# Kernel optimization log

Measured on AMD Instinct MI355X. Metric: run time of the kernel, lower is better.

## Reference

```python
import jax, jax.numpy as jnp
import numpy as np

EMBED_DIM = 1024
NUM_HEADS = 16
HEAD_DIM = EMBED_DIM // NUM_HEADS


def setup_inputs() -> dict:
    key = jax.random.key(0)
    ks = jax.random.split(key, 11)
    B, N, C = 2, 2048, EMBED_DIM
    s = 1.0 / np.sqrt(C)
    return {
        "query": jax.random.normal(ks[0], (B, N, C), jnp.float32),
        "key": jax.random.normal(ks[1], (B, N, C), jnp.float32),
        "value": jax.random.normal(ks[2], (B, N, C), jnp.float32),
        # torch nn.Linear weights: [out_features, in_features]
        "Wq": jax.random.normal(ks[3], (C, C), jnp.float32) * s,
        "bq": jnp.zeros((C,), jnp.float32),
        "Wk": jax.random.normal(ks[4], (C, C), jnp.float32) * s,
        "bk": jnp.zeros((C,), jnp.float32),
        "Wv": jax.random.normal(ks[5], (C, C), jnp.float32) * s,
        "bv": jnp.zeros((C,), jnp.float32),
        "Wo": jax.random.normal(ks[6], (C, C), jnp.float32) * s,
        "bo": jnp.zeros((C,), jnp.float32),
    }


def reference(query, key, value, Wq, bq, Wk, bk, Wv, bv, Wo, bo):
    B, N, C = query.shape
    H, D = NUM_HEADS, HEAD_DIM
    # projections (torch Linear: x @ W.T + b)
    q = query @ Wq.T + bq
    k = key @ Wk.T + bk
    v = value @ Wv.T + bv
    # [B, N, C] -> [B, H, N, D]
    q = q.reshape(B, N, H, D).transpose(0, 2, 1, 3)
    k = k.reshape(B, N, H, D).transpose(0, 2, 1, 3)
    v = v.reshape(B, N, H, D).transpose(0, 2, 1, 3)
    # scores: [B, H, N, N]
    scores = jnp.einsum("bhqd,bhkd->bhqk", q, k) / jnp.sqrt(jnp.asarray(D, q.dtype))
    attn = jax.nn.softmax(scores, axis=-1)
    # attend: [B, H, N, D] -> [B, N, C]
    out = jnp.einsum("bhqk,bhkd->bhqd", attn, v)
    out = out.transpose(0, 2, 1, 3).reshape(B, N, C)
    return out @ Wo.T + bo
```

## Files before the change

kernel.cpp:

```cpp
#include <hip/hip_runtime.h>
#include <hip/hip_bf16.h>
#include <cstdint>

typedef short bf16x8 __attribute__((ext_vector_type(8)));
typedef float f32x4 __attribute__((ext_vector_type(4)));
typedef float f32x16 __attribute__((ext_vector_type(16)));
typedef uint32_t u32x4v __attribute__((ext_vector_type(4)));
typedef unsigned short u16;

#define BATCH 2
#define NTOK 2048
#define CDIM 1024
#define NHEAD 16
#define DHEAD 64
#define MROWS 4096
#define KDIM 1024
#define KVB 128
#define NT (NTOK / KVB)

__device__ __forceinline__ uint32_t packbf2(float lo, float hi) {
    float2 f; f.x = lo; f.y = hi;
    __hip_bfloat162 h = __float22bfloat162_rn(f);
    uint32_t r;
    __builtin_memcpy(&r, &h, 4);
    return r;
}

__device__ __forceinline__ u16 f2bf(float x) {
    return (u16)(packbf2(x, 0.f) & 0xffffu);
}

__device__ __forceinline__ void gload_lds16(const void* g, void* l) {
    __builtin_amdgcn_global_load_lds((const __attribute__((address_space(1))) void*)g,
                                     (__attribute__((address_space(3))) void*)l,
                                     16, 0, 0);
}

__global__ __launch_bounds__(256) void cast_kernel(
    const float* __restrict__ q, const float* __restrict__ k, const float* __restrict__ v,
    const float* __restrict__ wq, const float* __restrict__ wk, const float* __restrict__ wv,
    const float* __restrict__ wo, u16* __restrict__ dst) {
    const size_t TOT = 16u << 20;
    size_t i0 = ((size_t)blockIdx.x * 256 + threadIdx.x) * 4;
    size_t stride = (size_t)gridDim.x * 256 * 4;
    for (size_t i = i0; i < TOT; i += stride) {
        const float* src;
        size_t off = i;
        if (i < (4u << 20))        { src = q;  }
        else if (i < (8u << 20))   { src = k;  off = i - (4u << 20); }
        else if (i < (12u << 20))  { src = v;  off = i - (8u << 20); }
        else if (i < (13u << 20))  { src = wq; off = i - (12u << 20); }
        else if (i < (14u << 20))  { src = wk; off = i - (13u << 20); }
        else if (i < (15u << 20))  { src = wv; off = i - (14u << 20); }
        else                       { src = wo; off = i - (15u << 20); }
        float4 f = *(const float4*)(src + off);
        uint2 packed;
        packed.x = packbf2(f.x, f.y);
        packed.y = packbf2(f.z, f.w);
        *(uint2*)(dst + i) = packed;
    }
}

__global__ __launch_bounds__(256, 3) void gemm_qkv(
    const u16* __restrict__ Xq, const u16* __restrict__ Xk, const u16* __restrict__ Xv,
    const u16* __restrict__ Wq, const u16* __restrict__ Wk, const u16* __restrict__ Wv,
    const float* __restrict__ bq, const float* __restrict__ bk, const float* __restrict__ bv,
    u16* __restrict__ Qo, u16* __restrict__ Ko, u16* __restrict__ Vo) {
    __shared__ u16 sA[128 * 32];
    __shared__ u16 sB[128 * 32];
    const int tid = threadIdx.x;
    const int lane = tid & 63;
    const int wave = tid >> 6;
    const int z = blockIdx.z;
    const u16* A  = (z == 0) ? Xq : (z == 1) ? Xk : Xv;
    const u16* Bw = (z == 0) ? Wq : (z == 1) ? Wk : Wv;
    const float* bias = (z == 0) ? bq : (z == 1) ? bk : bv;
    u16* Out = (z == 0) ? Qo : (z == 1) ? Ko : Vo;
    const float scale = (z == 0) ? 0.125f * 1.44269504088896f : 1.0f;

    const int m0 = blockIdx.x * 128, n0 = blockIdx.y * 128;
    const int wm = (wave >> 1) * 64, wn = (wave & 1) * 64;
    f32x4 acc[4][4] = {};
    const int rsel = lane & 15;
    const int ksel = (lane >> 4) * 8;

    for (int k0 = 0; k0 < KDIM; k0 += 32) {
#pragma unroll
        for (int u = 0; u < 2; ++u) {
            int c = tid + u * 256;
            int row = c >> 2, cin = c & 3;
            gload_lds16(A + (size_t)(m0 + row) * KDIM + k0 + cin * 8, &sA[c * 8]);
            gload_lds16(Bw + (size_t)(n0 + row) * KDIM + k0 + cin * 8, &sB[c * 8]);
        }
        __syncthreads();
        bf16x8 af[4], bfr[4];
#pragma unroll
        for (int i = 0; i < 4; ++i)
            af[i] = *(const bf16x8*)&sA[(wm + i * 16 + rsel) * 32 + ksel];
#pragma unroll
        for (int j = 0; j < 4; ++j)
            bfr[j] = *(const bf16x8*)&sB[(wn + j * 16 + rsel) * 32 + ksel];
#pragma unroll
        for (int i = 0; i < 4; ++i)
#pragma unroll
            for (int j = 0; j < 4; ++j)
                acc[i][j] = __builtin_amdgcn_mfma_f32_16x16x32_bf16(af[i], bfr[j], acc[i][j], 0, 0, 0);
        __syncthreads();
    }

    if (z != 2) {
#pragma unroll
        for (int i = 0; i < 4; ++i) {
            int mbase = m0 + wm + i * 16 + (lane >> 4) * 4;
#pragma unroll
            for (int j = 0; j < 4; ++j) {
                int n = n0 + wn + j * 16 + (lane & 15);
                float bv2 = bias[n];
                int h = n >> 6, d = n & 63;
#pragma unroll
                for (int r = 0; r < 4; ++r) {
                    int m = mbase + r;
                    int b = m >> 11, tok = m & 2047;
                    Out[(((size_t)(b * NHEAD + h)) * NTOK + tok) * DHEAD + d] =
                        f2bf((acc[i][j][r] + bv2) * scale);
                }
            }
        }
    } else {
#pragma unroll
        for (int i = 0; i < 4; ++i) {
            int mbase = m0 + wm + i * 16 + (lane >> 4) * 4;
            int b = mbase >> 11, tok = mbase & 2047;
#pragma unroll
            for (int j = 0; j < 4; ++j) {
                int n = n0 + wn + j * 16 + (lane & 15);
                float bv2 = bias[n];
                int h = n >> 6, d = n & 63;
                uint2 st;
                st.x = packbf2(acc[i][j][0] + bv2, acc[i][j][1] + bv2);
                st.y = packbf2(acc[i][j][2] + bv2, acc[i][j][3] + bv2);
                *(uint2*)&Out[(((size_t)(b * NHEAD + h)) * DHEAD + d) * NTOK + tok] = st;
            }
        }
    }
}

__global__ __launch_bounds__(256, 3) void gemm_out(
    const u16* __restrict__ A,
    const u16* __restrict__ Bw,
    const float* __restrict__ bias,
    float* __restrict__ Out,
    int M, int N, int K) {
    __shared__ u16 sA[128 * 32];
    __shared__ u16 sB[128 * 32];
    const int tid = threadIdx.x;
    const int lane = tid & 63;
    const int wave = tid >> 6;
    const int m0 = blockIdx.x * 128, n0 = blockIdx.y * 128;
    const int wm = (wave >> 1) * 64, wn = (wave & 1) * 64;
    f32x4 acc[4][4] = {};
    const int rsel = lane & 15;
    const int ksel = (lane >> 4) * 8;

    for (int k0 = 0; k0 < K; k0 += 32) {
#pragma unroll
        for (int u = 0; u < 2; ++u) {
            int c = tid + u * 256;
            int row = c >> 2, cin = c & 3;
            gload_lds16(A + (size_t)(m0 + row) * K + k0 + cin * 8, &sA[c * 8]);
            gload_lds16(Bw + (size_t)(n0 + row) * K + k0 + cin * 8, &sB[c * 8]);
        }
        __syncthreads();
        bf16x8 af[4], bfr[4];
#pragma unroll
        for (int i = 0; i < 4; ++i)
            af[i] = *(const bf16x8*)&sA[(wm + i * 16 + rsel) * 32 + ksel];
#pragma unroll
        for (int j = 0; j < 4; ++j)
            bfr[j] = *(const bf16x8*)&sB[(wn + j * 16 + rsel) * 32 + ksel];
#pragma unroll
        for (int i = 0; i < 4; ++i)
#pragma unroll
            for (int j = 0; j < 4; ++j)
                acc[i][j] = __builtin_amdgcn_mfma_f32_16x16x32_bf16(af[i], bfr[j], acc[i][j], 0, 0, 0);
        __syncthreads();
    }

#pragma unroll
    for (int i = 0; i < 4; ++i) {
        int mbase = m0 + wm + i * 16 + (lane >> 4) * 4;
#pragma unroll
        for (int j = 0; j < 4; ++j) {
            int n = n0 + wn + j * 16 + (lane & 15);
            float bv = bias[n];
#pragma unroll
            for (int r = 0; r < 4; ++r) {
                int m = mbase + r;
                Out[(size_t)m * N + n] = acc[i][j][r] + bv;
            }
        }
    }
}

__global__ __launch_bounds__(256, 2) void attn_kernel(
    const u16* __restrict__ Qg, const u16* __restrict__ Kg, const u16* __restrict__ Vg,
    u16* __restrict__ Og) {
    __shared__ u16 Ks[2][KVB * 64];
    __shared__ u16 Vt[2][64 * KVB];
    const int tid = threadIdx.x, lane = tid & 63, wave = tid >> 6;
    const int hi = lane >> 5, lq = lane & 31;

    int flat = blockIdx.x;
    int vflat = (flat & 7) * 64 + (flat >> 3);
    int bh = vflat >> 4;
    int qtile = vflat & 15;

    const int h = bh & (NHEAD - 1), b = bh >> 4;
    const u16* Qh = Qg + (size_t)bh * NTOK * DHEAD;
    const u16* Kh = Kg + (size_t)bh * NTOK * DHEAD;
    const u16* VhT = Vg + (size_t)bh * DHEAD * NTOK;
    const int qrow0 = qtile * 128 + wave * 32;
    const int qr = qrow0 + lq;

    bf16x8 qf[4];
#pragma unroll
    for (int dk = 0; dk < 4; ++dk)
        qf[dk] = *(const bf16x8*)&Qh[(size_t)qr * DHEAD + dk * 16 + hi * 8];

    f32x16 acc0 = {}, acc1 = {};
    f32x16 lacc = {};
    const bf16x8 ones = { (short)0x3F80, (short)0x3F80, (short)0x3F80, (short)0x3F80,
                          (short)0x3F80, (short)0x3F80, (short)0x3F80, (short)0x3F80 };

    const int pr = ((lq >> 2) & 1) * 8 + (lq & 3) + ((lq >> 3) & 1) * 4 + (lq >> 4) * 16;

    {
#pragma unroll
        for (int u = 0; u < 4; ++u) {
            int c2 = tid + u * 256;
            int kv = c2 >> 3, gi = c2 & 7;
            gload_lds16(Kh + (size_t)kv * DHEAD + (gi ^ (kv & 7)) * 8, &Ks[0][c2 * 8]);
        }
#pragma unroll
        for (int u = 0; u < 4; ++u) {
            int c2 = tid + u * 256;
            int d = c2 >> 4, gi = c2 & 15;
            gload_lds16(VhT + (size_t)d * NTOK + (gi ^ (d & 15)) * 8, &Vt[0][c2 * 8]);
        }
    }
    __syncthreads();

    int cur = 0;
    for (int t = 0; t < NT; ++t) {
        const bool pre = (t + 1 < NT);
        if (pre) {
#pragma unroll
            for (int u = 0; u < 4; ++u) {
                int c2 = tid + u * 256;
                int kv = c2 >> 3, gi = c2 & 7;
                gload_lds16(Kh + (size_t)((t + 1) * KVB + kv) * DHEAD + (gi ^ (kv & 7)) * 8,
                            &Ks[cur ^ 1][c2 * 8]);
            }
#pragma unroll
            for (int u = 0; u < 4; ++u) {
                int c2 = tid + u * 256;
                int d = c2 >> 4, gi = c2 & 15;
                gload_lds16(VhT + (size_t)d * NTOK + (t + 1) * KVB + (gi ^ (d & 15)) * 8,
                            &Vt[cur ^ 1][c2 * 8]);
            }
        }

        const char* kb_ = (const char*)&Ks[cur][0];
        bf16x8 pf[8];
#pragma unroll
        for (int j = 0; j < 4; ++j) {
            f32x16 T = {};
            int kv = j * 32 + pr;
            const char* kr = kb_ + kv * 128;
            int sx = (kv & 7) << 4;
#pragma unroll
            for (int dk = 0; dk < 4; ++dk) {
                bf16x8 kf = *(const bf16x8*)(kr + ((dk * 32 + hi * 16) ^ sx));
                T = __builtin_amdgcn_mfma_f32_32x32x16_bf16(kf, qf[dk], T, 0, 0, 0);
            }
#pragma unroll
            for (int i = 0; i < 16; ++i) T[i] = __builtin_amdgcn_exp2f(T[i]);
            u32x4v w0 = { packbf2(T[0], T[1]),  packbf2(T[2], T[3]),
                          packbf2(T[4], T[5]),  packbf2(T[6], T[7]) };
            u32x4v w1 = { packbf2(T[8], T[9]),  packbf2(T[10], T[11]),
                          packbf2(T[12], T[13]), packbf2(T[14], T[15]) };
            pf[j * 2]     = *(bf16x8*)&w0;
            pf[j * 2 + 1] = *(bf16x8*)&w1;
        }

        const char* vb_ = (const char*)&Vt[cur][0];
        __builtin_amdgcn_s_setprio(1);
#pragma unroll
        for (int db = 0; db < 2; ++db) {
            int d = db * 32 + lq;
#pragma unroll
            for (int ks = 0; ks < 8; ++ks) {
                int off = d * 256 + ((ks * 32 + hi * 16) ^ ((d & 15) << 4));
                bf16x8 vf = *(const bf16x8*)(vb_ + off);
                if (db == 0)
                    acc0 = __builtin_amdgcn_mfma_f32_32x32x16_bf16(vf, pf[ks], acc0, 0, 0, 0);
                else
                    acc1 = __builtin_amdgcn_mfma_f32_32x32x16_bf16(vf, pf[ks], acc1, 0, 0, 0);
            }
        }
#pragma unroll
        for (int ks = 0; ks < 8; ++ks)
            lacc = __builtin_amdgcn_mfma_f32_32x32x16_bf16(ones, pf[ks], lacc, 0, 0, 0);
        __builtin_amdgcn_s_setprio(0);

        __syncthreads();
        cur ^= 1;
    }

    float rinv = 1.0f / lacc[0];
#pragma unroll
    for (int db = 0; db < 2; ++db) {
#pragma unroll
        for (int rq = 0; rq < 4; ++rq) {
            int based = db * 32 + 8 * rq + 4 * hi;
            float o0, o1, o2, o3;
            if (db == 0) {
                o0 = acc0[rq * 4 + 0]; o1 = acc0[rq * 4 + 1];
                o2 = acc0[rq * 4 + 2]; o3 = acc0[rq * 4 + 3];
            } else {
                o0 = acc1[rq * 4 + 0]; o1 = acc1[rq * 4 + 1];
                o2 = acc1[rq * 4 + 2]; o3 = acc1[rq * 4 + 3];
            }
            uint2 st;
            st.x = packbf2(o0 * rinv, o1 * rinv);
            st.y = packbf2(o2 * rinv, o3 * rinv);
            *(uint2*)&Og[((size_t)(b * NTOK + qr)) * CDIM + h * DHEAD + based] = st;
        }
    }
}

extern "C" void kernel_launch(void* const* d_in, const int* in_sizes, int n_in,
                              void* d_out, int out_size, void* d_ws, size_t ws_size,
                              hipStream_t stream) {
    const float* q  = (const float*)d_in[0];
    const float* k  = (const float*)d_in[1];
    const float* v  = (const float*)d_in[2];
    const float* Wq = (const float*)d_in[3];
    const float* bq = (const float*)d_in[4];
    const float* Wk = (const float*)d_in[5];
    const float* bk = (const float*)d_in[6];
    const float* Wv = (const float*)d_in[7];
    const float* bv = (const float*)d_in[8];
    const float* Wo = (const float*)d_in[9];
    const float* bo = (const float*)d_in[10];

    u16* wsp = (u16*)d_ws;
    u16* Xq  = wsp;
    u16* Xk  = Xq + (4u << 20);
    u16* Xv  = Xk + (4u << 20);
    u16* Wqb = Xv + (4u << 20);
    u16* Wkb = Wqb + (1u << 20);
    u16* Wvb = Wkb + (1u << 20);
    u16* Wob = Wvb + (1u << 20);
    u16* Qb  = Wob + (1u << 20);
    u16* Kb  = Qb + (4u << 20);
    u16* Vb  = Kb + (4u << 20);
    u16* Ab  = Xq;

    cast_kernel<<<2048, 256, 0, stream>>>(q, k, v, Wq, Wk, Wv, Wo, Xq);

    gemm_qkv<<<dim3(MROWS / 128, CDIM / 128, 3), 256, 0, stream>>>(
        Xq, Xk, Xv, Wqb, Wkb, Wvb, bq, bk, bv, Qb, Kb, Vb);

    attn_kernel<<<512, 256, 0, stream>>>(Qb, Kb, Vb, Ab);

    gemm_out<<<dim3(MROWS / 128, CDIM / 128), 256, 0, stream>>>(
        Ab, Wob, bo, (float*)d_out, MROWS, CDIM, KDIM);
}
```

Measured before the change: 125.3 us.

## Switch attention to 16x16x32 MFMA with 64-row tiles and 64-key blocks

The attention kernel moves from 32x32x16 to 16x16x32 MFMA tiles. Each wave now handles 16 query rows instead of 32, the KV block shrinks from 128 to 64, and the grid doubles to 1024 blocks. The LDS swizzles are reworked to match, and launch bounds ask for 4 blocks per CU. This aims for more parallelism and occupancy with less register and LDS pressure per block, at the cost of more K/V reloads per query and more barriers per key sweep.

```diff
diff --git a/kernel.cpp b/kernel.cpp
--- a/kernel.cpp
+++ b/kernel.cpp
@@ -4,7 +4,6 @@
 
 typedef short bf16x8 __attribute__((ext_vector_type(8)));
 typedef float f32x4 __attribute__((ext_vector_type(4)));
-typedef float f32x16 __attribute__((ext_vector_type(16)));
 typedef uint32_t u32x4v __attribute__((ext_vector_type(4)));
 typedef unsigned short u16;
 
@@ -15,7 +14,7 @@
 #define DHEAD 64
 #define MROWS 4096
 #define KDIM 1024
-#define KVB 128
+#define KVB 64
 #define NT (NTOK / KVB)
 
 __device__ __forceinline__ uint32_t packbf2(float lo, float hi) {
@@ -202,50 +201,49 @@
     }
 }
 
-__global__ __launch_bounds__(256, 2) void attn_kernel(
+__global__ __launch_bounds__(256, 4) void attn_kernel(
     const u16* __restrict__ Qg, const u16* __restrict__ Kg, const u16* __restrict__ Vg,
     u16* __restrict__ Og) {
     __shared__ u16 Ks[2][KVB * 64];
     __shared__ u16 Vt[2][64 * KVB];
     const int tid = threadIdx.x, lane = tid & 63, wave = tid >> 6;
-    const int hi = lane >> 5, lq = lane & 31;
+    const int g = lane >> 4, m_ = lane & 15;
 
     int flat = blockIdx.x;
-    int vflat = (flat & 7) * 64 + (flat >> 3);
-    int bh = vflat >> 4;
-    int qtile = vflat & 15;
+    int vflat = (flat & 7) * 128 + (flat >> 3);
+    int bh = vflat >> 5;
+    int qtile = vflat & 31;
 
     const int h = bh & (NHEAD - 1), b = bh >> 4;
     const u16* Qh = Qg + (size_t)bh * NTOK * DHEAD;
     const u16* Kh = Kg + (size_t)bh * NTOK * DHEAD;
     const u16* VhT = Vg + (size_t)bh * DHEAD * NTOK;
-    const int qrow0 = qtile * 128 + wave * 32;
-    const int qr = qrow0 + lq;
-
-    bf16x8 qf[4];
-#pragma unroll
-    for (int dk = 0; dk < 4; ++dk)
-        qf[dk] = *(const bf16x8*)&Qh[(size_t)qr * DHEAD + dk * 16 + hi * 8];
-
-    f32x16 acc0 = {}, acc1 = {};
-    f32x16 lacc = {};
+    const int qrow0 = qtile * 64 + wave * 16;
+    const int qr = qrow0 + m_;
+
+    bf16x8 qf[2];
+#pragma unroll
+    for (int ks = 0; ks < 2; ++ks)
+        qf[ks] = *(const bf16x8*)&Qh[(size_t)qr * DHEAD + ks * 32 + g * 8];
+
+    f32x4 acc[4] = {};
+    f32x4 lacc = {};
     const bf16x8 ones = { (short)0x3F80, (short)0x3F80, (short)0x3F80, (short)0x3F80,
                           (short)0x3F80, (short)0x3F80, (short)0x3F80, (short)0x3F80 };
 
-    const int pr = ((lq >> 2) & 1) * 8 + (lq & 3) + ((lq >> 3) & 1) * 4 + (lq >> 4) * 16;
-
     {
 #pragma unroll
-        for (int u = 0; u < 4; ++u) {
+        for (int u = 0; u < 2; ++u) {
             int c2 = tid + u * 256;
             int kv = c2 >> 3, gi = c2 & 7;
-            gload_lds16(Kh + (size_t)kv * DHEAD + (gi ^ (kv & 7)) * 8, &Ks[0][c2 * 8]);
-        }
-#pragma unroll
-        for (int u = 0; u < 4; ++u) {
+            int fk = (kv & 3) | (((kv >> 3) & 1) << 2);
+            gload_lds16(Kh + (size_t)kv * DHEAD + (gi ^ fk) * 8, &Ks[0][c2 * 8]);
+        }
+#pragma unroll
+        for (int u = 0; u < 2; ++u) {
             int c2 = tid + u * 256;
-            int d = c2 >> 4, gi = c2 & 15;
-            gload_lds16(VhT + (size_t)d * NTOK + (gi ^ (d & 15)) * 8, &Vt[0][c2 * 8]);
+            int d = c2 >> 3, gi = c2 & 7;
+            gload_lds16(VhT + (size_t)d * NTOK + (gi ^ (d & 7)) * 8, &Vt[0][c2 * 8]);
         }
     }
     __syncthreads();
@@ -255,62 +253,63 @@
         const bool pre = (t + 1 < NT);
         if (pre) {
 #pragma unroll
-            for (int u = 0; u < 4; ++u) {
+            for (int u = 0; u < 2; ++u) {
                 int c2 = tid + u * 256;
                 int kv = c2 >> 3, gi = c2 & 7;
-                gload_lds16(Kh + (size_t)((t + 1) * KVB + kv) * DHEAD + (gi ^ (kv & 7)) * 8,
+                int fk = (kv & 3) | (((kv >> 3) & 1) << 2);
+                gload_lds16(Kh + (size_t)((t + 1) * KVB + kv) * DHEAD + (gi ^ fk) * 8,
                             &Ks[cur ^ 1][c2 * 8]);
             }
 #pragma unroll
-            for (int u = 0; u < 4; ++u) {
+            for (int u = 0; u < 2; ++u) {
                 int c2 = tid + u * 256;
-                int d = c2 >> 4, gi = c2 & 15;
-                gload_lds16(VhT + (size_t)d * NTOK + (t + 1) * KVB + (gi ^ (d & 15)) * 8,
+                int d = c2 >> 3, gi = c2 & 7;
+                gload_lds16(VhT + (size_t)d * NTOK + (t + 1) * KVB + (gi ^ (d & 7)) * 8,
                             &Vt[cur ^ 1][c2 * 8]);
             }
         }
 
         const char* kb_ = (const char*)&Ks[cur][0];
-        bf16x8 pf[8];
-#pragma unroll
-        for (int j = 0; j < 4; ++j) {
-            f32x16 T = {};
-            int kv = j * 32 + pr;
-            const char* kr = kb_ + kv * 128;
-            int sx = (kv & 7) << 4;
-#pragma unroll
-            for (int dk = 0; dk < 4; ++dk) {
-                bf16x8 kf = *(const bf16x8*)(kr + ((dk * 32 + hi * 16) ^ sx));
-                T = __builtin_amdgcn_mfma_f32_32x32x16_bf16(kf, qf[dk], T, 0, 0, 0);
-            }
-#pragma unroll
-            for (int i = 0; i < 16; ++i) T[i] = __builtin_amdgcn_exp2f(T[i]);
-            u32x4v w0 = { packbf2(T[0], T[1]),  packbf2(T[2], T[3]),
-                          packbf2(T[4], T[5]),  packbf2(T[6], T[7]) };
-            u32x4v w1 = { packbf2(T[8], T[9]),  packbf2(T[10], T[11]),
-                          packbf2(T[12], T[13]), packbf2(T[14], T[15]) };
-            pf[j * 2]     = *(bf16x8*)&w0;
-            pf[j * 2 + 1] = *(bf16x8*)&w1;
+        bf16x8 pf[2];
+        __builtin_amdgcn_s_setprio(1);
+#pragma unroll
+        for (int c = 0; c < 2; ++c) {
+            f32x4 Tt[2];
+#pragma unroll
+            for (int t2 = 0; t2 < 2; ++t2) {
+                int tau = c * 2 + t2;
+                int kv = (tau >> 1) * 32 + ((m_ >> 2) & 3) * 8 + ((tau & 1) << 2) + (m_ & 3);
+                int fk = (kv & 3) | (((kv >> 3) & 1) << 2);
+                f32x4 T = {};
+#pragma unroll
+                for (int ks = 0; ks < 2; ++ks) {
+                    int oct = (ks * 4 + g) ^ fk;
+                    bf16x8 kf = *(const bf16x8*)(kb_ + kv * 128 + oct * 16);
+                    T = __builtin_amdgcn_mfma_f32_16x16x32_bf16(kf, qf[ks], T, 0, 0, 0);
+                }
+#pragma unroll
+                for (int i = 0; i < 4; ++i) T[i] = __builtin_amdgcn_exp2f(T[i]);
+                Tt[t2] = T;
+            }
+            u32x4v w = { packbf2(Tt[0][0], Tt[0][1]), packbf2(Tt[0][2], Tt[0][3]),
+                         packbf2(Tt[1][0], Tt[1][1]), packbf2(Tt[1][2], Tt[1][3]) };
+            pf[c] = *(bf16x8*)&w;
         }
 
         const char* vb_ = (const char*)&Vt[cur][0];
-        __builtin_amdgcn_s_setprio(1);
-#pragma unroll
-        for (int db = 0; db < 2; ++db) {
-            int d = db * 32 + lq;
-#pragma unroll
-            for (int ks = 0; ks < 8; ++ks) {
-                int off = d * 256 + ((ks * 32 + hi * 16) ^ ((d & 15) << 4));
-                bf16x8 vf = *(const bf16x8*)(vb_ + off);
-                if (db == 0)
-                    acc0 = __builtin_amdgcn_mfma_f32_32x32x16_bf16(vf, pf[ks], acc0, 0, 0, 0);
-                else
-                    acc1 = __builtin_amdgcn_mfma_f32_32x32x16_bf16(vf, pf[ks], acc1, 0, 0, 0);
-            }
-        }
-#pragma unroll
-        for (int ks = 0; ks < 8; ++ks)
-            lacc = __builtin_amdgcn_mfma_f32_32x32x16_bf16(ones, pf[ks], lacc, 0, 0, 0);
+#pragma unroll
+        for (int dt = 0; dt < 4; ++dt) {
+            int d = dt * 16 + m_;
+#pragma unroll
+            for (int c = 0; c < 2; ++c) {
+                int oct = (c * 4 + g) ^ (d & 7);
+                bf16x8 vf = *(const bf16x8*)(vb_ + d * 128 + oct * 16);
+                acc[dt] = __builtin_amdgcn_mfma_f32_16x16x32_bf16(vf, pf[c], acc[dt], 0, 0, 0);
+            }
+        }
+#pragma unroll
+        for (int c = 0; c < 2; ++c)
+            lacc = __builtin_amdgcn_mfma_f32_16x16x32_bf16(ones, pf[c], lacc, 0, 0, 0);
         __builtin_amdgcn_s_setprio(0);
 
         __syncthreads();
@@ -319,23 +318,12 @@
 
     float rinv = 1.0f / lacc[0];
 #pragma unroll
-    for (int db = 0; db < 2; ++db) {
-#pragma unroll
-        for (int rq = 0; rq < 4; ++rq) {
-            int based = db * 32 + 8 * rq + 4 * hi;
-            float o0, o1, o2, o3;
-            if (db == 0) {
-                o0 = acc0[rq * 4 + 0]; o1 = acc0[rq * 4 + 1];
-                o2 = acc0[rq * 4 + 2]; o3 = acc0[rq * 4 + 3];
-            } else {
-                o0 = acc1[rq * 4 + 0]; o1 = acc1[rq * 4 + 1];
-                o2 = acc1[rq * 4 + 2]; o3 = acc1[rq * 4 + 3];
-            }
-            uint2 st;
-            st.x = packbf2(o0 * rinv, o1 * rinv);
-            st.y = packbf2(o2 * rinv, o3 * rinv);
-            *(uint2*)&Og[((size_t)(b * NTOK + qr)) * CDIM + h * DHEAD + based] = st;
-        }
+    for (int dt = 0; dt < 4; ++dt) {
+        int dbase = dt * 16 + g * 4;
+        uint2 st;
+        st.x = packbf2(acc[dt][0] * rinv, acc[dt][1] * rinv);
+        st.y = packbf2(acc[dt][2] * rinv, acc[dt][3] * rinv);
+        *(uint2*)&Og[((size_t)(b * NTOK + qr)) * CDIM + h * DHEAD + dbase] = st;
     }
 }
 
@@ -372,7 +360,7 @@
     gemm_qkv<<<dim3(MROWS / 128, CDIM / 128, 3), 256, 0, stream>>>(
         Xq, Xk, Xv, Wqb, Wkb, Wvb, bq, bk, bv, Qb, Kb, Vb);
 
-    attn_kernel<<<512, 256, 0, stream>>>(Qb, Kb, Vb, Ab);
+    attn_kernel<<<1024, 256, 0, stream>>>(Qb, Kb, Vb, Ab);
 
     gemm_out<<<dim3(MROWS / 128, CDIM / 128), 256, 0, stream>>>(
         Ab, Wob, bo, (float*)d_out, MROWS, CDIM, KDIM);
```

After: 126.0 us. No clear change (+0.6%).

## Read K and V fragments directly from global memory, dropping LDS staging

Applied to the files above, without the earlier changes.

The attention kernel no longer stages K and transposed V tiles through double-buffered shared memory. Each wave now loads its MFMA operands straight from global memory, which removes the LDS buffers, the swizzling and the per-tile barriers. Every one of the four waves re-reads the same K/V tile from global or L2, so redundant traffic rises and load latency is no longer hidden by the prefetch double buffer. Removing the LDS use may allow more blocks per CU.

```diff
diff --git a/kernel.cpp b/kernel.cpp
--- a/kernel.cpp
+++ b/kernel.cpp
@@ -205,8 +205,6 @@
 __global__ __launch_bounds__(256, 2) void attn_kernel(
     const u16* __restrict__ Qg, const u16* __restrict__ Kg, const u16* __restrict__ Vg,
     u16* __restrict__ Og) {
-    __shared__ u16 Ks[2][KVB * 64];
-    __shared__ u16 Vt[2][64 * KVB];
     const int tid = threadIdx.x, lane = tid & 63, wave = tid >> 6;
     const int hi = lane >> 5, lq = lane & 31;
 
@@ -234,53 +232,24 @@
 
     const int pr = ((lq >> 2) & 1) * 8 + (lq & 3) + ((lq >> 3) & 1) * 4 + (lq >> 4) * 16;
 
-    {
-#pragma unroll
-        for (int u = 0; u < 4; ++u) {
-            int c2 = tid + u * 256;
-            int kv = c2 >> 3, gi = c2 & 7;
-            gload_lds16(Kh + (size_t)kv * DHEAD + (gi ^ (kv & 7)) * 8, &Ks[0][c2 * 8]);
-        }
-#pragma unroll
-        for (int u = 0; u < 4; ++u) {
-            int c2 = tid + u * 256;
-            int d = c2 >> 4, gi = c2 & 15;
-            gload_lds16(VhT + (size_t)d * NTOK + (gi ^ (d & 15)) * 8, &Vt[0][c2 * 8]);
-        }
-    }
-    __syncthreads();
-
-    int cur = 0;
+    const u16* Kbase = Kh + pr * DHEAD + hi * 8;
+    const u16* Vbase0 = VhT + (size_t)lq * NTOK + hi * 8;
+    const u16* Vbase1 = VhT + (size_t)(32 + lq) * NTOK + hi * 8;
+
     for (int t = 0; t < NT; ++t) {
-        const bool pre = (t + 1 < NT);
-        if (pre) {
-#pragma unroll
-            for (int u = 0; u < 4; ++u) {
-                int c2 = tid + u * 256;
-                int kv = c2 >> 3, gi = c2 & 7;
-                gload_lds16(Kh + (size_t)((t + 1) * KVB + kv) * DHEAD + (gi ^ (kv & 7)) * 8,
-                            &Ks[cur ^ 1][c2 * 8]);
-            }
-#pragma unroll
-            for (int u = 0; u < 4; ++u) {
-                int c2 = tid + u * 256;
-                int d = c2 >> 4, gi = c2 & 15;
-                gload_lds16(VhT + (size_t)d * NTOK + (t + 1) * KVB + (gi ^ (d & 15)) * 8,
-                            &Vt[cur ^ 1][c2 * 8]);
-            }
-        }
-
-        const char* kb_ = (const char*)&Ks[cur][0];
+        const u16* Kt = Kbase + (size_t)t * KVB * DHEAD;
+        const u16* Vt0 = Vbase0 + t * KVB;
+        const u16* Vt1 = Vbase1 + t * KVB;
+
         bf16x8 pf[8];
+        __builtin_amdgcn_s_setprio(1);
 #pragma unroll
         for (int j = 0; j < 4; ++j) {
             f32x16 T = {};
-            int kv = j * 32 + pr;
-            const char* kr = kb_ + kv * 128;
-            int sx = (kv & 7) << 4;
+            const u16* kr = Kt + j * 32 * DHEAD;
 #pragma unroll
             for (int dk = 0; dk < 4; ++dk) {
-                bf16x8 kf = *(const bf16x8*)(kr + ((dk * 32 + hi * 16) ^ sx));
+                bf16x8 kf = *(const bf16x8*)(kr + dk * 16);
                 T = __builtin_amdgcn_mfma_f32_32x32x16_bf16(kf, qf[dk], T, 0, 0, 0);
             }
 #pragma unroll
@@ -293,28 +262,17 @@
             pf[j * 2 + 1] = *(bf16x8*)&w1;
         }
 
-        const char* vb_ = (const char*)&Vt[cur][0];
-        __builtin_amdgcn_s_setprio(1);
-#pragma unroll
-        for (int db = 0; db < 2; ++db) {
-            int d = db * 32 + lq;
-#pragma unroll
-            for (int ks = 0; ks < 8; ++ks) {
-                int off = d * 256 + ((ks * 32 + hi * 16) ^ ((d & 15) << 4));
-                bf16x8 vf = *(const bf16x8*)(vb_ + off);
-                if (db == 0)
-                    acc0 = __builtin_amdgcn_mfma_f32_32x32x16_bf16(vf, pf[ks], acc0, 0, 0, 0);
-                else
-                    acc1 = __builtin_amdgcn_mfma_f32_32x32x16_bf16(vf, pf[ks], acc1, 0, 0, 0);
-            }
+#pragma unroll
+        for (int ks = 0; ks < 8; ++ks) {
+            bf16x8 vf0 = *(const bf16x8*)(Vt0 + ks * 16);
+            bf16x8 vf1 = *(const bf16x8*)(Vt1 + ks * 16);
+            acc0 = __builtin_amdgcn_mfma_f32_32x32x16_bf16(vf0, pf[ks], acc0, 0, 0, 0);
+            acc1 = __builtin_amdgcn_mfma_f32_32x32x16_bf16(vf1, pf[ks], acc1, 0, 0, 0);
         }
 #pragma unroll
         for (int ks = 0; ks < 8; ++ks)
             lacc = __builtin_amdgcn_mfma_f32_32x32x16_bf16(ones, pf[ks], lacc, 0, 0, 0);
         __builtin_amdgcn_s_setprio(0);
-
-        __syncthreads();
-        cur ^= 1;
     }
 
     float rinv = 1.0f / lacc[0];
```

New measurement: 202.3 us. +61.4%, slower.
